# Optimization experiments

Measured on AMD Instinct MI355X. Metric: run time of the kernel, lower is better.

The kernel has to match this reference:

```python
import jax, jax.numpy as jnp
import numpy as np

B, D_IN, D_H = 16384, 512, 1024


def _glorot(key, out_d, in_d):
    lim = 1.0 / np.sqrt(in_d)
    return jax.random.uniform(key, (out_d, in_d), minval=-lim, maxval=lim, dtype=jnp.float32)


def setup_inputs() -> dict:
    key = jax.random.key(0)
    ks = jax.random.split(key, 16)
    inp = {
        "x_t": jax.random.normal(ks[0], (B, D_IN), dtype=jnp.float32),
        "delta_t": jax.random.uniform(ks[1], (B, 1), dtype=jnp.float32),
        "h_prev": jax.random.normal(ks[2], (B, D_H), dtype=jnp.float32),
        # torch nn.Linear weights are [out, in]; y = x @ W.T
        "W_sh": _glorot(ks[3], D_H, D_H),
        "W_sx": _glorot(ks[4], D_H, D_IN),
        "W_st": _glorot(ks[5], D_H, 1),
        "b_s": jnp.zeros((D_H,), jnp.float32),
        "WTh": _glorot(ks[6], D_H, D_H),
        "WTx": _glorot(ks[7], D_H, D_IN),
        "WTs": _glorot(ks[8], D_H, D_H),
        "b_T": jnp.zeros((D_H,), jnp.float32),
        "W_rh": _glorot(ks[9], D_H, D_H),
        "W_rx": _glorot(ks[10], D_H, D_IN),
        "b_r": jnp.zeros((D_H,), jnp.float32),
        "W_zh": _glorot(ks[11], D_H, D_H),
        "W_zx": _glorot(ks[12], D_H, D_IN),
        "b_z": jnp.zeros((D_H,), jnp.float32),
        "W_h": _glorot(ks[13], D_H, D_H),
        "W_x": _glorot(ks[14], D_H, D_IN),
        "b": jnp.zeros((D_H,), jnp.float32),
    }
    return inp


def reference(x_t, delta_t, h_prev,
              W_sh, W_sx, W_st, b_s,
              WTh, WTx, WTs, b_T,
              W_rh, W_rx, b_r,
              W_zh, W_zx, b_z,
              W_h, W_x, b):
    lin = lambda x, W: x @ W.T  # nn.Linear(bias=False)
    s_t = jnp.tanh(lin(h_prev, W_sh) + lin(x_t, W_sx) + lin(delta_t, W_st) + b_s)
    T_t = jax.nn.sigmoid(lin(h_prev, WTh) + lin(x_t, WTx) + lin(s_t, WTs) + b_T)
    r_t = jax.nn.sigmoid(lin(h_prev, W_rh) + lin(x_t, W_rx) + b_r)
    z_t = jax.nn.sigmoid(lin(h_prev, W_zh) + lin(x_t, W_zx) + b_z)
    h_tilde = jnp.tanh(lin(r_t * h_prev, W_h) + lin(x_t, W_x) + b)
    h_t = (1.0 - z_t) * (T_t * h_prev) + z_t * h_tilde
    return h_t
```

## Files before the change

### kernel.cpp

```cpp
#include <hip/hip_runtime.h>
#include <stdint.h>

#define AS1 __attribute__((address_space(1)))
#define AS3 __attribute__((address_space(3)))

typedef unsigned short US;
typedef __bf16 bf16x8 __attribute__((ext_vector_type(8)));
typedef float f32x4 __attribute__((ext_vector_type(4)));

static constexpr int Bsz = 16384;
static constexpr int DIN = 512;
static constexpr int DH  = 1024;
static constexpr int LDA = 1536;

__device__ __forceinline__ US f2bf(float f) {
  unsigned u = __float_as_uint(f);
  u += 0x7fffu + ((u >> 16) & 1u);
  return (US)(u >> 16);
}
__device__ __forceinline__ float bf2f(US u) { return __uint_as_float(((unsigned)u) << 16); }
__device__ __forceinline__ float sigm(float x) { return 1.f / (1.f + __expf(-x)); }
__device__ __forceinline__ float tanh_f(float x) { return 1.f - 2.f / (1.f + __expf(2.f * x)); }

__global__ void pack_A(const float* __restrict__ h, const float* __restrict__ x,
                       US* __restrict__ Ab) {
  const int total = Bsz * 384;
  for (int idx = blockIdx.x * blockDim.x + threadIdx.x; idx < total;
       idx += gridDim.x * blockDim.x) {
    int row = idx / 384;
    int c = (idx - row * 384) * 4;
    const float* src = (c < DH) ? (h + (size_t)row * DH + c)
                                : (x + (size_t)row * DIN + (c - DH));
    float4 v = *(const float4*)src;
    ushort4 o;
    o.x = f2bf(v.x); o.y = f2bf(v.y); o.z = f2bf(v.z); o.w = f2bf(v.w);
    *(ushort4*)(Ab + (size_t)row * LDA + c) = o;
  }
}

struct WSlot { const float* src; US* dst; int n4; };
struct WBatch { WSlot s[11]; };
__global__ void conv_w(WBatch b) {
  WSlot sl = b.s[blockIdx.y];
  for (int i = blockIdx.x * blockDim.x + threadIdx.x; i < sl.n4;
       i += gridDim.x * blockDim.x) {
    float4 v = *(const float4*)(sl.src + (size_t)i * 4);
    ushort4 o;
    o.x = f2bf(v.x); o.y = f2bf(v.y); o.z = f2bf(v.z); o.w = f2bf(v.w);
    *(ushort4*)(sl.dst + (size_t)i * 4) = o;
  }
}

template <int EPI, int KT0, int KT1, int KT2>
__global__ __launch_bounds__(256) void gemm_ep(
    const US* __restrict__ A0, int lda0,
    const US* __restrict__ A1, int lda1,
    const US* __restrict__ A2, int lda2,
    const US* __restrict__ W0, int ldw0,
    const US* __restrict__ W1, int ldw1,
    const US* __restrict__ W2, int ldw2,
    const float* __restrict__ bias,
    const void* aux0, const void* aux1, const void* aux2,
    void* outp, int ldo) {
  __shared__ __align__(16) US As[128 * 64];
  __shared__ __align__(16) US Bs[128 * 64];

  const int tid  = threadIdx.x;
  const int lane = tid & 63;
  const int w    = tid >> 6;

  const int p = blockIdx.x + (int)(gridDim.x * blockIdx.y);
  const int c = p & 7;
  const int q = p >> 3;
  const int nIdx = q & 7;
  const int mIdx = c * 16 + (q >> 3);
  const int mBase = mIdx * 128;
  const int nBase = nIdx * 128;

  f32x4 acc[4][4];
#pragma unroll
  for (int i = 0; i < 4; i++)
#pragma unroll
    for (int j = 0; j < 4; j++) acc[i][j] = f32x4{0.f, 0.f, 0.f, 0.f};

  const int rowL = w * 32 + (lane >> 3);
  const int cc   = lane & 7;
  const int scc  = cc ^ ((lane >> 3) & 7);
  const int gOff = scc * 8;
  const int wm = (w & 1) * 64, wn = (w >> 1) * 64;
  const int quad = lane >> 4, l15 = lane & 15;
  const int sw = l15 & 7;

#define K_TILE_LOOP(Ap, lda, Wp, ldw, KT)                                          \
  {                                                                                \
    const US* ga = (Ap) + (size_t)(mBase + rowL) * (lda) + gOff;                   \
    const US* gw = (Wp) + (size_t)(nBase + rowL) * (ldw) + gOff;                   \
    const size_t a8 = (size_t)8 * (lda), w8 = (size_t)8 * (ldw);                   \
    for (int k = 0; k < (KT); ++k) {                                               \
      _Pragma("unroll")                                                            \
      for (int i = 0; i < 4; i++) {                                                \
        __builtin_amdgcn_global_load_lds((AS1 const void*)(ga + i * a8),           \
            (AS3 void*)&As[(w * 32 + i * 8) * 64], 16, 0, 0);                      \
        __builtin_amdgcn_global_load_lds((AS1 const void*)(gw + i * w8),           \
            (AS3 void*)&Bs[(w * 32 + i * 8) * 64], 16, 0, 0);                      \
      }                                                                            \
      __builtin_amdgcn_s_waitcnt(0x0f70);                                          \
      __syncthreads();                                                             \
      _Pragma("unroll")                                                            \
      for (int ks = 0; ks < 2; ++ks) {                                             \
        bf16x8 af[4], bw[4];                                                       \
        _Pragma("unroll")                                                          \
        for (int i = 0; i < 4; i++)                                                \
          af[i] = *(const bf16x8*)&As[(wm + i * 16 + l15) * 64 +                   \
                                      (((ks * 4 + quad) ^ sw) * 8)];               \
        _Pragma("unroll")                                                          \
        for (int j = 0; j < 4; j++)                                                \
          bw[j] = *(const bf16x8*)&Bs[(wn + j * 16 + l15) * 64 +                   \
                                      (((ks * 4 + quad) ^ sw) * 8)];               \
        _Pragma("unroll")                                                          \
        for (int i = 0; i < 4; i++)                                                \
          _Pragma("unroll")                                                        \
          for (int j = 0; j < 4; j++)                                              \
            acc[i][j] = __builtin_amdgcn_mfma_f32_16x16x32_bf16(af[i], bw[j],      \
                                                                acc[i][j], 0, 0, 0);\
      }                                                                            \
      __syncthreads();                                                             \
      ga += 64; gw += 64;                                                          \
    }                                                                              \
  }

  if constexpr (KT0 > 0) K_TILE_LOOP(A0, lda0, W0, ldw0, KT0);
  if constexpr (KT1 > 0) K_TILE_LOOP(A1, lda1, W1, ldw1, KT1);
  if constexpr (KT2 > 0) K_TILE_LOOP(A2, lda2, W2, ldw2, KT2);
#undef K_TILE_LOOP

#pragma unroll
  for (int i = 0; i < 4; i++) {
#pragma unroll
    for (int j = 0; j < 4; j++) {
      const int col = nBase + wn + j * 16 + l15;
      const float bv = bias[col];
#pragma unroll
      for (int r = 0; r < 4; r++) {
        const int row = mBase + wm + i * 16 + quad * 4 + r;
        float v = acc[i][j][r] + bv;
        if constexpr (EPI == 0) {
          const float* delta = (const float*)aux0;
          const float* wst   = (const float*)aux1;
          v += delta[row] * wst[col];
          ((US*)outp)[(size_t)row * ldo + col] = f2bf(tanh_f(v));
        } else if constexpr (EPI == 1) {
          const float* hp = (const float*)aux0;
          float rr = sigm(v);
          ((US*)outp)[(size_t)row * ldo + col] =
              f2bf(rr * hp[(size_t)row * DH + col]);
        } else if constexpr (EPI == 2) {
          ((US*)outp)[(size_t)row * ldo + col] = f2bf(sigm(v));
        } else if constexpr (EPI == 3) {
          ((US*)outp)[(size_t)row * ldo + col] = f2bf(tanh_f(v));
        } else {
          const float* hp = (const float*)aux0;
          const US* Zp = (const US*)aux1;
          const US* Hp = (const US*)aux2;
          float T = sigm(v);
          size_t o = (size_t)row * DH + col;
          float z = bf2f(Zp[o]), ht = bf2f(Hp[o]);
          float h = hp[o];
          ((float*)outp)[(size_t)row * ldo + col] = (1.f - z) * (T * h) + z * ht;
        }
      }
    }
  }
}

extern "C" void kernel_launch(void* const* d_in, const int* in_sizes, int n_in,
                              void* d_out, int out_size, void* d_ws, size_t ws_size,
                              hipStream_t stream) {
  const float* x_t   = (const float*)d_in[0];
  const float* delta = (const float*)d_in[1];
  const float* h_prev= (const float*)d_in[2];
  const float* W_sh  = (const float*)d_in[3];
  const float* W_sx  = (const float*)d_in[4];
  const float* W_st  = (const float*)d_in[5];
  const float* b_s   = (const float*)d_in[6];
  const float* WTh   = (const float*)d_in[7];
  const float* WTx   = (const float*)d_in[8];
  const float* WTs   = (const float*)d_in[9];
  const float* b_T   = (const float*)d_in[10];
  const float* W_rh  = (const float*)d_in[11];
  const float* W_rx  = (const float*)d_in[12];
  const float* b_r   = (const float*)d_in[13];
  const float* W_zh  = (const float*)d_in[14];
  const float* W_zx  = (const float*)d_in[15];
  const float* b_z   = (const float*)d_in[16];
  const float* W_h   = (const float*)d_in[17];
  const float* W_x   = (const float*)d_in[18];
  const float* b_    = (const float*)d_in[19];
  float* out = (float*)d_out;

  char* ws = (char*)d_ws;
  US* Ab = (US*)ws;                         size_t off = (size_t)Bsz * LDA * 2;
  US* Sb = (US*)(ws + off);                 off += (size_t)Bsz * DH * 2;
  US* RH = (US*)(ws + off);                 off += (size_t)Bsz * DH * 2;
  US* Zb = (US*)(ws + off);                 off += (size_t)Bsz * DH * 2;
  US* HTb = (US*)(ws + off);                off += (size_t)Bsz * DH * 2;
  const size_t WHH = (size_t)DH * DH * 2, WHX = (size_t)DH * DIN * 2;
  US* bWsh = (US*)(ws + off); off += WHH;
  US* bWsx = (US*)(ws + off); off += WHX;
  US* bWTh = (US*)(ws + off); off += WHH;
  US* bWTx = (US*)(ws + off); off += WHX;
  US* bWTs = (US*)(ws + off); off += WHH;
  US* bWrh = (US*)(ws + off); off += WHH;
  US* bWrx = (US*)(ws + off); off += WHX;
  US* bWzh = (US*)(ws + off); off += WHH;
  US* bWzx = (US*)(ws + off); off += WHX;
  US* bWh  = (US*)(ws + off); off += WHH;
  US* bWx  = (US*)(ws + off); off += WHX;

  pack_A<<<dim3(8192), 256, 0, stream>>>(h_prev, x_t, Ab);
  WBatch wb;
  const int n4h = DH * DH / 4, n4x = DH * DIN / 4;
  wb.s[0]  = {W_sh, bWsh, n4h};  wb.s[1]  = {W_sx, bWsx, n4x};
  wb.s[2]  = {WTh,  bWTh, n4h};  wb.s[3]  = {WTx,  bWTx, n4x};
  wb.s[4]  = {WTs,  bWTs, n4h};  wb.s[5]  = {W_rh, bWrh, n4h};
  wb.s[6]  = {W_rx, bWrx, n4x};  wb.s[7]  = {W_zh, bWzh, n4h};
  wb.s[8]  = {W_zx, bWzx, n4x};  wb.s[9]  = {W_h,  bWh,  n4h};
  wb.s[10] = {W_x,  bWx,  n4x};
  conv_w<<<dim3(512, 11), 256, 0, stream>>>(wb);

  dim3 grid(DH / 128, Bsz / 128);
  const US* A_h = Ab;
  const US* A_x = Ab + DH;

  gemm_ep<0, 16, 8, 0><<<grid, 256, 0, stream>>>(
      A_h, LDA, A_x, LDA, nullptr, 0,
      bWsh, DH, bWsx, DIN, nullptr, 0,
      b_s, delta, W_st, nullptr, (void*)Sb, DH);
  gemm_ep<1, 16, 8, 0><<<grid, 256, 0, stream>>>(
      A_h, LDA, A_x, LDA, nullptr, 0,
      bWrh, DH, bWrx, DIN, nullptr, 0,
      b_r, h_prev, nullptr, nullptr, (void*)RH, DH);
  gemm_ep<2, 16, 8, 0><<<grid, 256, 0, stream>>>(
      A_h, LDA, A_x, LDA, nullptr, 0,
      bWzh, DH, bWzx, DIN, nullptr, 0,
      b_z, nullptr, nullptr, nullptr, (void*)Zb, DH);
  gemm_ep<3, 16, 8, 0><<<grid, 256, 0, stream>>>(
      RH, DH, A_x, LDA, nullptr, 0,
      bWh, DH, bWx, DIN, nullptr, 0,
      b_, nullptr, nullptr, nullptr, (void*)HTb, DH);
  gemm_ep<4, 16, 8, 16><<<grid, 256, 0, stream>>>(
      A_h, LDA, A_x, LDA, Sb, DH,
      bWTh, DH, bWTx, DIN, bWTs, DH,
      b_T, h_prev, Zb, HTb, (void*)out, DH);
}
```

Measured before the change: 655.5 us.

## Double-buffer LDS tiles and concatenate weights into single contiguous K loops

Adds a two-stage LDS double buffer so the global-to-LDS loads for the next K tile are issued before computing the current one, removing one barrier per tile and overlapping memory with MFMA work. Weights are packed into concatenated [N, K_total] matrices, and activations are laid out so that h, x and s (and r*h with x) sit side by side in one wide row. Each GEMM then becomes a single uniform K loop. The cost is double the LDS per block (32 KB), which may lower occupancy, plus extra copies of x into the RH buffer and wider strides in the packed activation array.

```diff
diff --git a/kernel.cpp b/kernel.cpp
--- a/kernel.cpp
+++ b/kernel.cpp
@@ -11,7 +11,8 @@
 static constexpr int Bsz = 16384;
 static constexpr int DIN = 512;
 static constexpr int DH  = 1024;
-static constexpr int LDA = 1536;
+static constexpr int LDA = 2560;
+static constexpr int LDR = 1536;
 
 __device__ __forceinline__ US f2bf(float f) {
   unsigned u = __float_as_uint(f);
@@ -23,7 +24,7 @@
 __device__ __forceinline__ float tanh_f(float x) { return 1.f - 2.f / (1.f + __expf(2.f * x)); }
 
 __global__ void pack_A(const float* __restrict__ h, const float* __restrict__ x,
-                       US* __restrict__ Ab) {
+                       US* __restrict__ Ab, US* __restrict__ RHx) {
   const int total = Bsz * 384;
   for (int idx = blockIdx.x * blockDim.x + threadIdx.x; idx < total;
        idx += gridDim.x * blockDim.x) {
@@ -35,43 +36,42 @@
     ushort4 o;
     o.x = f2bf(v.x); o.y = f2bf(v.y); o.z = f2bf(v.z); o.w = f2bf(v.w);
     *(ushort4*)(Ab + (size_t)row * LDA + c) = o;
-  }
-}
-
-struct WSlot { const float* src; US* dst; int n4; };
+    if (c >= DH) *(ushort4*)(RHx + (size_t)row * LDR + c) = o;
+  }
+}
+
+struct WSlot { const float* src; US* dst; int n4; int ksh; int ld; int co; };
 struct WBatch { WSlot s[11]; };
 __global__ void conv_w(WBatch b) {
   WSlot sl = b.s[blockIdx.y];
+  const int mask = (1 << sl.ksh) - 1;
   for (int i = blockIdx.x * blockDim.x + threadIdx.x; i < sl.n4;
        i += gridDim.x * blockDim.x) {
     float4 v = *(const float4*)(sl.src + (size_t)i * 4);
     ushort4 o;
     o.x = f2bf(v.x); o.y = f2bf(v.y); o.z = f2bf(v.z); o.w = f2bf(v.w);
-    *(ushort4*)(sl.dst + (size_t)i * 4) = o;
-  }
-}
-
-template <int EPI, int KT0, int KT1, int KT2>
+    int r = i >> sl.ksh;
+    int cc = (i & mask) * 4;
+    *(ushort4*)(sl.dst + (size_t)r * sl.ld + sl.co + cc) = o;
+  }
+}
+
+template <int EPI>
 __global__ __launch_bounds__(256) void gemm_ep(
-    const US* __restrict__ A0, int lda0,
-    const US* __restrict__ A1, int lda1,
-    const US* __restrict__ A2, int lda2,
-    const US* __restrict__ W0, int ldw0,
-    const US* __restrict__ W1, int ldw1,
-    const US* __restrict__ W2, int ldw2,
+    const US* __restrict__ A, int lda,
+    const US* __restrict__ W, int ldw, int nt,
     const float* __restrict__ bias,
     const void* aux0, const void* aux1, const void* aux2,
     void* outp, int ldo) {
-  __shared__ __align__(16) US As[128 * 64];
-  __shared__ __align__(16) US Bs[128 * 64];
+  __shared__ __align__(16) US As[2][128 * 64];
+  __shared__ __align__(16) US Bs[2][128 * 64];
 
   const int tid  = threadIdx.x;
   const int lane = tid & 63;
   const int w    = tid >> 6;
 
-  const int p = blockIdx.x + (int)(gridDim.x * blockIdx.y);
-  const int c = p & 7;
-  const int q = p >> 3;
+  const int p = blockIdx.x;
+  const int c = p & 7, q = p >> 3;
   const int nIdx = q & 7;
   const int mIdx = c * 16 + (q >> 3);
   const int mBase = mIdx * 128;
@@ -84,55 +84,58 @@
     for (int j = 0; j < 4; j++) acc[i][j] = f32x4{0.f, 0.f, 0.f, 0.f};
 
   const int rowL = w * 32 + (lane >> 3);
-  const int cc   = lane & 7;
-  const int scc  = cc ^ ((lane >> 3) & 7);
+  const int scc  = (lane & 7) ^ ((lane >> 3) & 7);
   const int gOff = scc * 8;
   const int wm = (w & 1) * 64, wn = (w >> 1) * 64;
   const int quad = lane >> 4, l15 = lane & 15;
   const int sw = l15 & 7;
 
-#define K_TILE_LOOP(Ap, lda, Wp, ldw, KT)                                          \
-  {                                                                                \
-    const US* ga = (Ap) + (size_t)(mBase + rowL) * (lda) + gOff;                   \
-    const US* gw = (Wp) + (size_t)(nBase + rowL) * (ldw) + gOff;                   \
-    const size_t a8 = (size_t)8 * (lda), w8 = (size_t)8 * (ldw);                   \
-    for (int k = 0; k < (KT); ++k) {                                               \
-      _Pragma("unroll")                                                            \
-      for (int i = 0; i < 4; i++) {                                                \
-        __builtin_amdgcn_global_load_lds((AS1 const void*)(ga + i * a8),           \
-            (AS3 void*)&As[(w * 32 + i * 8) * 64], 16, 0, 0);                      \
-        __builtin_amdgcn_global_load_lds((AS1 const void*)(gw + i * w8),           \
-            (AS3 void*)&Bs[(w * 32 + i * 8) * 64], 16, 0, 0);                      \
-      }                                                                            \
-      __builtin_amdgcn_s_waitcnt(0x0f70);                                          \
-      __syncthreads();                                                             \
-      _Pragma("unroll")                                                            \
-      for (int ks = 0; ks < 2; ++ks) {                                             \
-        bf16x8 af[4], bw[4];                                                       \
-        _Pragma("unroll")                                                          \
-        for (int i = 0; i < 4; i++)                                                \
-          af[i] = *(const bf16x8*)&As[(wm + i * 16 + l15) * 64 +                   \
-                                      (((ks * 4 + quad) ^ sw) * 8)];               \
-        _Pragma("unroll")                                                          \
-        for (int j = 0; j < 4; j++)                                                \
-          bw[j] = *(const bf16x8*)&Bs[(wn + j * 16 + l15) * 64 +                   \
-                                      (((ks * 4 + quad) ^ sw) * 8)];               \
-        _Pragma("unroll")                                                          \
-        for (int i = 0; i < 4; i++)                                                \
-          _Pragma("unroll")                                                        \
-          for (int j = 0; j < 4; j++)                                              \
-            acc[i][j] = __builtin_amdgcn_mfma_f32_16x16x32_bf16(af[i], bw[j],      \
-                                                                acc[i][j], 0, 0, 0);\
-      }                                                                            \
-      __syncthreads();                                                             \
-      ga += 64; gw += 64;                                                          \
-    }                                                                              \
-  }
-
-  if constexpr (KT0 > 0) K_TILE_LOOP(A0, lda0, W0, ldw0, KT0);
-  if constexpr (KT1 > 0) K_TILE_LOOP(A1, lda1, W1, ldw1, KT1);
-  if constexpr (KT2 > 0) K_TILE_LOOP(A2, lda2, W2, ldw2, KT2);
-#undef K_TILE_LOOP
+  const US* gaBase = A + (size_t)(mBase + rowL) * lda + gOff;
+  const US* gwBase = W + (size_t)(nBase + rowL) * ldw + gOff;
+  const size_t a8 = (size_t)8 * lda, w8 = (size_t)8 * ldw;
+
+#define STAGE(d, co)                                                             \
+  { const US* ga = gaBase + (co);                                                \
+    const US* gw = gwBase + (co);                                                \
+    _Pragma("unroll")                                                            \
+    for (int i = 0; i < 4; i++) {                                                \
+      __builtin_amdgcn_global_load_lds((AS1 const void*)(ga + i * a8),           \
+          (AS3 void*)&As[d][(w * 32 + i * 8) * 64], 16, 0, 0);                   \
+      __builtin_amdgcn_global_load_lds((AS1 const void*)(gw + i * w8),           \
+          (AS3 void*)&Bs[d][(w * 32 + i * 8) * 64], 16, 0, 0);                   \
+    } }
+
+#define COMPUTE(d)                                                               \
+  { _Pragma("unroll")                                                            \
+    for (int ks = 0; ks < 2; ++ks) {                                             \
+      bf16x8 af[4], bw[4];                                                       \
+      _Pragma("unroll")                                                          \
+      for (int i = 0; i < 4; i++)                                                \
+        af[i] = *(const bf16x8*)&As[d][(wm + i * 16 + l15) * 64 +                \
+                                       (((ks * 4 + quad) ^ sw) * 8)];            \
+      _Pragma("unroll")                                                          \
+      for (int j = 0; j < 4; j++)                                                \
+        bw[j] = *(const bf16x8*)&Bs[d][(wn + j * 16 + l15) * 64 +                \
+                                       (((ks * 4 + quad) ^ sw) * 8)];            \
+      _Pragma("unroll")                                                          \
+      for (int i = 0; i < 4; i++)                                                \
+        _Pragma("unroll")                                                        \
+        for (int j = 0; j < 4; j++)                                              \
+          acc[i][j] = __builtin_amdgcn_mfma_f32_16x16x32_bf16(af[i], bw[j],      \
+                                                              acc[i][j], 0, 0, 0);\
+    } }
+
+  STAGE(0, 0);
+  __syncthreads();
+
+  int cur = 0;
+  for (int t = 0; t < nt; ++t, cur ^= 1) {
+    if (t + 1 < nt) STAGE(cur ^ 1, (t + 1) * 64);
+    COMPUTE(cur);
+    __syncthreads();
+  }
+#undef STAGE
+#undef COMPUTE
 
 #pragma unroll
   for (int i = 0; i < 4; i++) {
@@ -199,57 +202,47 @@
   float* out = (float*)d_out;
 
   char* ws = (char*)d_ws;
-  US* Ab = (US*)ws;                         size_t off = (size_t)Bsz * LDA * 2;
-  US* Sb = (US*)(ws + off);                 off += (size_t)Bsz * DH * 2;
-  US* RH = (US*)(ws + off);                 off += (size_t)Bsz * DH * 2;
-  US* Zb = (US*)(ws + off);                 off += (size_t)Bsz * DH * 2;
-  US* HTb = (US*)(ws + off);                off += (size_t)Bsz * DH * 2;
-  const size_t WHH = (size_t)DH * DH * 2, WHX = (size_t)DH * DIN * 2;
-  US* bWsh = (US*)(ws + off); off += WHH;
-  US* bWsx = (US*)(ws + off); off += WHX;
-  US* bWTh = (US*)(ws + off); off += WHH;
-  US* bWTx = (US*)(ws + off); off += WHX;
-  US* bWTs = (US*)(ws + off); off += WHH;
-  US* bWrh = (US*)(ws + off); off += WHH;
-  US* bWrx = (US*)(ws + off); off += WHX;
-  US* bWzh = (US*)(ws + off); off += WHH;
-  US* bWzx = (US*)(ws + off); off += WHX;
-  US* bWh  = (US*)(ws + off); off += WHH;
-  US* bWx  = (US*)(ws + off); off += WHX;
-
-  pack_A<<<dim3(8192), 256, 0, stream>>>(h_prev, x_t, Ab);
+  US* Ab  = (US*)ws;              size_t off = (size_t)Bsz * LDA * 2;
+  US* RH  = (US*)(ws + off);      off += (size_t)Bsz * LDR * 2;
+  US* Zb  = (US*)(ws + off);      off += (size_t)Bsz * DH * 2;
+  US* HTb = (US*)(ws + off);      off += (size_t)Bsz * DH * 2;
+  US* bWsrz = (US*)(ws + off);    off += (size_t)3072 * 1536 * 2;
+  US* bWT   = (US*)(ws + off);    off += (size_t)DH * 2560 * 2;
+  US* bWh   = (US*)(ws + off);    off += (size_t)DH * 1536 * 2;
+
+  pack_A<<<dim3(8192), 256, 0, stream>>>(h_prev, x_t, Ab, RH);
   WBatch wb;
   const int n4h = DH * DH / 4, n4x = DH * DIN / 4;
-  wb.s[0]  = {W_sh, bWsh, n4h};  wb.s[1]  = {W_sx, bWsx, n4x};
-  wb.s[2]  = {WTh,  bWTh, n4h};  wb.s[3]  = {WTx,  bWTx, n4x};
-  wb.s[4]  = {WTs,  bWTs, n4h};  wb.s[5]  = {W_rh, bWrh, n4h};
-  wb.s[6]  = {W_rx, bWrx, n4x};  wb.s[7]  = {W_zh, bWzh, n4h};
-  wb.s[8]  = {W_zx, bWzx, n4x};  wb.s[9]  = {W_h,  bWh,  n4h};
-  wb.s[10] = {W_x,  bWx,  n4x};
+  US* bWr = bWsrz + (size_t)1024 * 1536;
+  US* bWz = bWsrz + (size_t)2048 * 1536;
+  wb.s[0]  = {W_sh, bWsrz, n4h, 8, 1536, 0};
+  wb.s[1]  = {W_sx, bWsrz, n4x, 7, 1536, 1024};
+  wb.s[2]  = {W_rh, bWr,   n4h, 8, 1536, 0};
+  wb.s[3]  = {W_rx, bWr,   n4x, 7, 1536, 1024};
+  wb.s[4]  = {W_zh, bWz,   n4h, 8, 1536, 0};
+  wb.s[5]  = {W_zx, bWz,   n4x, 7, 1536, 1024};
+  wb.s[6]  = {WTh,  bWT,   n4h, 8, 2560, 0};
+  wb.s[7]  = {WTx,  bWT,   n4x, 7, 2560, 1024};
+  wb.s[8]  = {WTs,  bWT,   n4h, 8, 2560, 1536};
+  wb.s[9]  = {W_h,  bWh,   n4h, 8, 1536, 0};
+  wb.s[10] = {W_x,  bWh,   n4x, 7, 1536, 1024};
   conv_w<<<dim3(512, 11), 256, 0, stream>>>(wb);
 
-  dim3 grid(DH / 128, Bsz / 128);
-  const US* A_h = Ab;
-  const US* A_x = Ab + DH;
-
-  gemm_ep<0, 16, 8, 0><<<grid, 256, 0, stream>>>(
-      A_h, LDA, A_x, LDA, nullptr, 0,
-      bWsh, DH, bWsx, DIN, nullptr, 0,
-      b_s, delta, W_st, nullptr, (void*)Sb, DH);
-  gemm_ep<1, 16, 8, 0><<<grid, 256, 0, stream>>>(
-      A_h, LDA, A_x, LDA, nullptr, 0,
-      bWrh, DH, bWrx, DIN, nullptr, 0,
-      b_r, h_prev, nullptr, nullptr, (void*)RH, DH);
-  gemm_ep<2, 16, 8, 0><<<grid, 256, 0, stream>>>(
-      A_h, LDA, A_x, LDA, nullptr, 0,
-      bWzh, DH, bWzx, DIN, nullptr, 0,
-      b_z, nullptr, nullptr, nullptr, (void*)Zb, DH);
-  gemm_ep<3, 16, 8, 0><<<grid, 256, 0, stream>>>(
-      RH, DH, A_x, LDA, nullptr, 0,
-      bWh, DH, bWx, DIN, nullptr, 0,
-      b_, nullptr, nullptr, nullptr, (void*)HTb, DH);
-  gemm_ep<4, 16, 8, 16><<<grid, 256, 0, stream>>>(
-      A_h, LDA, A_x, LDA, Sb, DH,
-      bWTh, DH, bWTx, DIN, bWTs, DH,
-      b_T, h_prev, Zb, HTb, (void*)out, DH);
-}
+  const dim3 grid(1024);
+
+  gemm_ep<0><<<grid, 256, 0, stream>>>(Ab, LDA, bWsrz, 1536, 24, b_s,
+                                       delta, W_st, nullptr,
+                                       (void*)(Ab + 1536), LDA);
+  gemm_ep<1><<<grid, 256, 0, stream>>>(Ab, LDA, bWr, 1536, 24, b_r,
+                                       h_prev, nullptr, nullptr,
+                                       (void*)RH, LDR);
+  gemm_ep<2><<<grid, 256, 0, stream>>>(Ab, LDA, bWz, 1536, 24, b_z,
+                                       nullptr, nullptr, nullptr,
+                                       (void*)Zb, DH);
+  gemm_ep<3><<<grid, 256, 0, stream>>>(RH, LDR, bWh, 1536, 24, b_,
+                                       nullptr, nullptr, nullptr,
+                                       (void*)HTb, DH);
+  gemm_ep<4><<<grid, 256, 0, stream>>>(Ab, LDA, bWT, 2560, 40, b_T,
+                                       h_prev, Zb, HTb,
+                                       (void*)out, DH);
+}
```

Result: faster. 642.0 us (-2.1%).
